# Kernel optimization log

Measured on AMD Instinct MI355X. Metric: run time of the kernel, lower is better.

Reference implementation:

```python
import jax, jax.numpy as jnp
import numpy as np

# geomloss SamplesLoss('sinkhorn', p=1, blur=0.01, reach=None, debias=True)
P = 1
EPS = 0.01  # temperature = blur**p
N_ITERS = 32
LOSS_WEIGHT = 1.0


def setup_inputs() -> dict:
    key = jax.random.key(0)
    kx, ky = jax.random.split(key)
    x = jax.random.normal(kx, (6144, 3), dtype=jnp.float32)
    y = jax.random.normal(ky, (6144, 3), dtype=jnp.float32)
    return {"x": x, "y": y}


def _cost(x, y):
    # p=1 cost: Euclidean distance ||x_i - y_j||, via expanded quadratic form
    x2 = jnp.sum(x * x, axis=-1)  # [N]
    y2 = jnp.sum(y * y, axis=-1)  # [M]
    d2 = x2[:, None] + y2[None, :] - 2.0 * (x @ y.T)  # [N, M]
    return jnp.sqrt(jnp.maximum(d2, 0.0) + 1e-12)


def _softmin(C, h):
    # h: [M] = log_weights + dual/eps ; returns [N] = -eps*LSE_j(h_j - C_ij/eps)
    return -EPS * jax.scipy.special.logsumexp(h[None, :] - C / EPS, axis=1)


def _sinkhorn_potentials(C_xy, loga, logb):
    # symmetric log-domain Sinkhorn with averaged updates (geomloss style)
    N, M = C_xy.shape
    f0 = jnp.zeros((N,), C_xy.dtype)
    g0 = jnp.zeros((M,), C_xy.dtype)

    def step(carry, _):
        f, g = carry
        ft = _softmin(C_xy, logb + g / EPS)
        gt = _softmin(C_xy.T, loga + f / EPS)
        return (0.5 * (f + ft), 0.5 * (g + gt)), None

    (f, g), _ = jax.lax.scan(step, (f0, g0), None, length=N_ITERS)
    # final non-averaged extrapolation step
    f_fin = _softmin(C_xy, logb + g / EPS)
    g_fin = _softmin(C_xy.T, loga + f / EPS)
    return f_fin, g_fin


def _sym_potential(C_xx, logw):
    # debias term: symmetric fixed point p = softmin(C_xx, logw + p/eps)
    N = C_xx.shape[0]

    def step(p, _):
        return 0.5 * (p + _softmin(C_xx, logw + p / EPS)), None

    p, _ = jax.lax.scan(step, jnp.zeros((N,), C_xx.dtype), None, length=N_ITERS)
    return _softmin(C_xx, logw + p / EPS)


def reference(x, y):
    N, M = x.shape[0], y.shape[0]
    a = jnp.full((N,), 1.0 / N, x.dtype)
    b = jnp.full((M,), 1.0 / M, y.dtype)
    loga = jnp.log(a)
    logb = jnp.log(b)

    C_xy = _cost(x, y)
    C_xx = _cost(x, x)
    C_yy = _cost(y, y)

    f, g = _sinkhorn_potentials(C_xy, loga, logb)
    p_x = _sym_potential(C_xx, loga)
    p_y = _sym_potential(C_yy, logb)

    # debiased Sinkhorn divergence: <a, f - p_x> + <b, g - p_y>
    loss = jnp.sum(a * (f - p_x)) + jnp.sum(b * (g - p_y))
    return LOSS_WEIGHT * loss
```

## Files before the change

### kernel.cpp

```cpp
#include <hip/hip_runtime.h>
#include <math.h>

#ifndef __has_builtin
#define __has_builtin(x) 0
#endif

__device__ __forceinline__ float fexp2(float x) {
#if __has_builtin(__builtin_amdgcn_exp2f)
  return __builtin_amdgcn_exp2f(x);
#else
  return exp2f(x);
#endif
}
__device__ __forceinline__ float flog2(float x) {
#if __has_builtin(__builtin_amdgcn_logf)
  return __builtin_amdgcn_logf(x);
#else
  return log2f(x);
#endif
}
__device__ __forceinline__ float fsqrt_(float x) {
#if __has_builtin(__builtin_amdgcn_sqrtf)
  return __builtin_amdgcn_sqrtf(x);
#else
  return sqrtf(x);
#endif
}

constexpr int   NP    = 6144;
constexpr float LOG2E = 1.44269504088896340736f;
constexpr float EPS_F = 0.01f;
constexpr float KKc   = LOG2E / EPS_F;
constexpr float NKKc  = -KKc;
constexpr float LBc   = -8.72323127482750f;
constexpr float HBc   = LBc * LOG2E;
constexpr float NEL2c = -EPS_F * 0.693147180559945f;

constexpr int TILE = 1024;
constexpr int NT   = NP / TILE;
constexpr int RPW  = 4;
constexpr int RPB  = 16;
constexpr int BPS  = NP / RPB;

__global__ __launch_bounds__(256) void init_kernel(
    const float* __restrict__ x, const float* __restrict__ y,
    float4* __restrict__ Xp, float4* __restrict__ Yp,
    float4* __restrict__ Xq, float4* __restrict__ Yq,
    float* __restrict__ st)
{
  int i = blockIdx.x * 256 + threadIdx.x;
  if (i < NP) {
    float a0 = x[3*i], a1 = x[3*i+1], a2 = x[3*i+2];
    float an = fmaf(a0, a0, fmaf(a1, a1, a2*a2));
    Xp[i] = make_float4(a0, a1, a2, an);
    Xq[i] = make_float4(-2.f*a0, -2.f*a1, -2.f*a2, an);
    float b0 = y[3*i], b1 = y[3*i+1], b2 = y[3*i+2];
    float bn = fmaf(b0, b0, fmaf(b1, b1, b2*b2));
    Yp[i] = make_float4(b0, b1, b2, bn);
    Yq[i] = make_float4(-2.f*b0, -2.f*b1, -2.f*b2, bn);
    st[i] = 0.f; st[i + NP] = 0.f; st[i + 2*NP] = 0.f; st[i + 3*NP] = 0.f;
  }
}

__global__ __launch_bounds__(256, 6) void softmin_pass(
    const float4* __restrict__ Xp, const float4* __restrict__ Yp,
    const float4* __restrict__ Xq, const float4* __restrict__ Yq,
    const float* __restrict__ f_in,  const float* __restrict__ g_in,
    const float* __restrict__ px_in, const float* __restrict__ py_in,
    float* __restrict__ f_out,  float* __restrict__ g_out,
    float* __restrict__ px_out, float* __restrict__ py_out,
    int avg)
{
  __shared__ float4 sQ[TILE];
  __shared__ float  sH[TILE];

  const int bid   = blockIdx.x;
  const int sub   = bid / BPS;
  const int row0  = (bid - sub * BPS) * RPB;
  const int tid   = threadIdx.x;
  const int lane  = tid & 63;
  const int wave  = tid >> 6;
  const int wrow0 = row0 + wave * RPW;

  const float4* P4;  const float4* Q4;
  const float* hsrc; const float* oldp; float* outp;
  if (sub == 0)      { P4 = Xp; Q4 = Yq; hsrc = g_in;  oldp = f_in;  outp = f_out;  }
  else if (sub == 1) { P4 = Yp; Q4 = Xq; hsrc = f_in;  oldp = g_in;  outp = g_out;  }
  else if (sub == 2) { P4 = Xp; Q4 = Xq; hsrc = px_in; oldp = px_in; outp = px_out; }
  else               { P4 = Yp; Q4 = Yq; hsrc = py_in; oldp = py_in; outp = py_out; }

  float pxr[RPW], pyr[RPW], pzr[RPW], pwr[RPW];
  float mr[RPW], sr[RPW], m40[RPW];
#pragma unroll
  for (int r = 0; r < RPW; ++r) {
    float4 p = P4[wrow0 + r];
    pxr[r] = p.x; pyr[r] = p.y; pzr[r] = p.z; pwr[r] = p.w;
    mr[r] = -INFINITY; sr[r] = 0.f; m40[r] = -INFINITY;
  }

  for (int t = 0; t < NT; ++t) {
    __syncthreads();
#pragma unroll
    for (int v = tid; v < TILE; v += 256) {
      sQ[v] = Q4[t * TILE + v];
      sH[v] = fmaf(KKc, hsrc[t * TILE + v], HBc);
    }
    __syncthreads();
#pragma unroll 4
    for (int k = lane; k < TILE; k += 64) {
      const float4 q  = sQ[k];
      const float  hh = sH[k];
#pragma unroll
      for (int r = 0; r < RPW; ++r) {
        float dot = fmaf(pxr[r], q.x, fmaf(pyr[r], q.y, fmaf(pzr[r], q.z, q.w)));
        float d2  = pwr[r] + dot;
        float c   = fsqrt_(fmaxf(d2, 1e-12f));
        float u   = fmaf(NKKc, c, hh);
        if (__any(u > m40[r])) {
          float mn = fmaxf(mr[r], u);
          sr[r] *= fexp2(mr[r] - mn);
          mr[r]  = mn;
          m40[r] = mn + 40.f;
        }
        sr[r] += fexp2(u - mr[r]);
      }
    }
  }

#pragma unroll
  for (int r = 0; r < RPW; ++r) {
    float m = mr[r], s = sr[r];
#pragma unroll
    for (int off = 32; off; off >>= 1) {
      float mo = __shfl_xor(m, off);
      float so = __shfl_xor(s, off);
      float mn = fmaxf(m, mo);
      s = s * fexp2(m - mn) + so * fexp2(mo - mn);
      m = mn;
    }
    if (lane == 0) {
      float val = NEL2c * (m + flog2(s));
      const int row = wrow0 + r;
      outp[row] = avg ? 0.5f * (oldp[row] + val) : val;
    }
  }
}

__global__ __launch_bounds__(256) void loss_kernel(
    const float* __restrict__ f,  const float* __restrict__ g,
    const float* __restrict__ px, const float* __restrict__ py,
    float* __restrict__ out)
{
  double acc = 0.0;
  for (int i = threadIdx.x; i < NP; i += 256)
    acc += (double)(f[i] - px[i]) + (double)(g[i] - py[i]);
  __shared__ double red[4];
#pragma unroll
  for (int off = 32; off; off >>= 1)
    acc += __shfl_xor(acc, off);
  const int lane = threadIdx.x & 63, wave = threadIdx.x >> 6;
  if (lane == 0) red[wave] = acc;
  __syncthreads();
  if (threadIdx.x == 0)
    out[0] = (float)((red[0] + red[1] + red[2] + red[3]) * (1.0 / NP));
}

extern "C" void kernel_launch(void* const* d_in, const int* in_sizes, int n_in,
                              void* d_out, int out_size, void* d_ws, size_t ws_size,
                              hipStream_t stream)
{
  const float* x = (const float*)d_in[0];
  const float* y = (const float*)d_in[1];
  float* out = (float*)d_out;
  float* ws  = (float*)d_ws;

  float4* Xp = (float4*)ws;
  float4* Yp = (float4*)(ws + 4 * NP);
  float4* Xq = (float4*)(ws + 8 * NP);
  float4* Yq = (float4*)(ws + 12 * NP);
  float* A = ws + 16 * NP;
  float* B = A + 4 * NP;

  hipLaunchKernelGGL(init_kernel, dim3((NP + 255) / 256), dim3(256), 0, stream,
                     x, y, Xp, Yp, Xq, Yq, A);

  float* cur = A; float* nxt = B;
  for (int it = 0; it <= 32; ++it) {
    const int avg = (it < 32) ? 1 : 0;
    hipLaunchKernelGGL(softmin_pass, dim3(4 * BPS), dim3(256), 0, stream,
                       Xp, Yp, Xq, Yq,
                       cur, cur + NP, cur + 2*NP, cur + 3*NP,
                       nxt, nxt + NP, nxt + 2*NP, nxt + 3*NP, avg);
    float* t = cur; cur = nxt; nxt = t;
  }

  hipLaunchKernelGGL(loss_kernel, dim3(1), dim3(256), 0, stream,
                     cur, cur + NP, cur + 2*NP, cur + 3*NP, out);
}
```

Baseline: 2.561 ms.

## Morton-sort points and skip far tiles using bounding-box softmin bounds

Points are spatially sorted into Morton order with a single-block counting sort, and a per-64-point bounding box is computed for each tile. Each softmin block computes lower and upper bounds on the exponent for every tile, using box distances and per-row-block maxima of the previous potentials. Tiles whose best possible contribution is more than 2^-40 below the guaranteed maximum are skipped. This cuts exp and sqrt work on distant pairs. It trades that for a bounded approximation error, a serial two-block sort kernel, loss of LDS tiling, and the risk of stale hmax bounds from the previous iteration.

Result: faster. 2.385 ms (-6.9%).

```diff
diff --git a/kernel.cpp b/kernel.cpp
--- a/kernel.cpp
+++ b/kernel.cpp
@@ -36,97 +36,197 @@
 constexpr float HBc   = LBc * LOG2E;
 constexpr float NEL2c = -EPS_F * 0.693147180559945f;
 
-constexpr int TILE = 1024;
-constexpr int NT   = NP / TILE;
-constexpr int RPW  = 4;
-constexpr int RPB  = 16;
-constexpr int BPS  = NP / RPB;
-
-__global__ __launch_bounds__(256) void init_kernel(
-    const float* __restrict__ x, const float* __restrict__ y,
-    float4* __restrict__ Xp, float4* __restrict__ Yp,
-    float4* __restrict__ Xq, float4* __restrict__ Yq,
-    float* __restrict__ st)
+constexpr int RPW  = 8;
+constexpr int RPB  = 32;
+constexpr int NRB  = NP / RPB;
+constexpr int NTL  = NP / 64;
+constexpr int CELLS = 4096;
+
+__device__ __forceinline__ unsigned cell_of(float v) {
+  int c = (int)floorf((v + 4.0f) * 2.0f);
+  return (unsigned)min(15, max(0, c));
+}
+__device__ __forceinline__ unsigned morton12(unsigned cx, unsigned cy, unsigned cz) {
+  unsigned m = 0;
+#pragma unroll
+  for (int b = 0; b < 4; ++b)
+    m |= (((cx >> b) & 1u) << (3 * b)) | (((cy >> b) & 1u) << (3 * b + 1)) |
+         (((cz >> b) & 1u) << (3 * b + 2));
+  return m;
+}
+
+__global__ __launch_bounds__(1024) void sort_kernel(
+    const float* __restrict__ xin, const float* __restrict__ yin,
+    float4* __restrict__ Xp, float4* __restrict__ Xq,
+    float4* __restrict__ Yp, float4* __restrict__ Yq,
+    float4* __restrict__ XaLo, float4* __restrict__ XaHi,
+    float4* __restrict__ YaLo, float4* __restrict__ YaHi,
+    float* __restrict__ stA, float* __restrict__ hmaxA)
 {
-  int i = blockIdx.x * 256 + threadIdx.x;
-  if (i < NP) {
-    float a0 = x[3*i], a1 = x[3*i+1], a2 = x[3*i+2];
-    float an = fmaf(a0, a0, fmaf(a1, a1, a2*a2));
-    Xp[i] = make_float4(a0, a1, a2, an);
-    Xq[i] = make_float4(-2.f*a0, -2.f*a1, -2.f*a2, an);
-    float b0 = y[3*i], b1 = y[3*i+1], b2 = y[3*i+2];
-    float bn = fmaf(b0, b0, fmaf(b1, b1, b2*b2));
-    Yp[i] = make_float4(b0, b1, b2, bn);
-    Yq[i] = make_float4(-2.f*b0, -2.f*b1, -2.f*b2, bn);
-    st[i] = 0.f; st[i + NP] = 0.f; st[i + 2*NP] = 0.f; st[i + 3*NP] = 0.f;
-  }
-}
-
-__global__ __launch_bounds__(256, 6) void softmin_pass(
+  __shared__ unsigned hist[CELLS];
+  __shared__ unsigned offs[CELLS];
+  __shared__ unsigned wsum[64];
+  const int tid = threadIdx.x;
+  const float* src = (blockIdx.x == 0) ? xin : yin;
+  float4* Pp  = (blockIdx.x == 0) ? Xp : Yp;
+  float4* Pq  = (blockIdx.x == 0) ? Xq : Yq;
+  float4* aLo = (blockIdx.x == 0) ? XaLo : YaLo;
+  float4* aHi = (blockIdx.x == 0) ? XaHi : YaHi;
+
+  for (int i = tid; i < CELLS; i += 1024) { hist[i] = 0u; offs[i] = 0u; }
+  for (int i = tid; i < 2 * NP; i += 1024) stA[blockIdx.x * 2 * NP + i] = 0.f;
+  for (int i = tid; i < 2 * NRB; i += 1024) hmaxA[blockIdx.x * 2 * NRB + i] = 0.f;
+  __syncthreads();
+
+  for (int i = tid; i < NP; i += 1024) {
+    float a0 = src[3*i], a1 = src[3*i+1], a2 = src[3*i+2];
+    unsigned m = morton12(cell_of(a0), cell_of(a1), cell_of(a2));
+    atomicAdd(&hist[m], 1u);
+  }
+  __syncthreads();
+  if (tid < 64) {
+    unsigned s = 0;
+    for (int j = 0; j < 64; ++j) { unsigned v = hist[tid*64+j]; hist[tid*64+j] = s; s += v; }
+    wsum[tid] = s;
+  }
+  __syncthreads();
+  if (tid == 0) {
+    unsigned s = 0;
+    for (int j = 0; j < 64; ++j) { unsigned v = wsum[j]; wsum[j] = s; s += v; }
+  }
+  __syncthreads();
+  if (tid < 64) {
+    unsigned o = wsum[tid];
+    for (int j = 0; j < 64; ++j) hist[tid*64+j] += o;
+  }
+  __syncthreads();
+  for (int i = tid; i < NP; i += 1024) {
+    float a0 = src[3*i], a1 = src[3*i+1], a2 = src[3*i+2];
+    unsigned m = morton12(cell_of(a0), cell_of(a1), cell_of(a2));
+    unsigned dst = hist[m] + atomicAdd(&offs[m], 1u);
+    float an = fmaf(a0, a0, fmaf(a1, a1, a2 * a2));
+    Pp[dst] = make_float4(a0, a1, a2, an);
+    Pq[dst] = make_float4(-2.f*a0, -2.f*a1, -2.f*a2, an);
+  }
+  __syncthreads();
+  const int wave = tid >> 6, lane = tid & 63;
+  for (int t = wave; t < NTL; t += 16) {
+    float4 p = Pp[t * 64 + lane];
+    float lx = p.x, ly = p.y, lz = p.z, hx = p.x, hy = p.y, hz = p.z;
+#pragma unroll
+    for (int off = 32; off; off >>= 1) {
+      lx = fminf(lx, __shfl_xor(lx, off)); hx = fmaxf(hx, __shfl_xor(hx, off));
+      ly = fminf(ly, __shfl_xor(ly, off)); hy = fmaxf(hy, __shfl_xor(hy, off));
+      lz = fminf(lz, __shfl_xor(lz, off)); hz = fmaxf(hz, __shfl_xor(hz, off));
+    }
+    if (lane == 0) {
+      aLo[t] = make_float4(lx, ly, lz, 0.f);
+      aHi[t] = make_float4(hx, hy, hz, 0.f);
+    }
+  }
+}
+
+__global__ __launch_bounds__(256, 4) void softmin_pass(
     const float4* __restrict__ Xp, const float4* __restrict__ Yp,
     const float4* __restrict__ Xq, const float4* __restrict__ Yq,
-    const float* __restrict__ f_in,  const float* __restrict__ g_in,
-    const float* __restrict__ px_in, const float* __restrict__ py_in,
-    float* __restrict__ f_out,  float* __restrict__ g_out,
-    float* __restrict__ px_out, float* __restrict__ py_out,
-    int avg)
+    const float4* __restrict__ XaLo, const float4* __restrict__ XaHi,
+    const float4* __restrict__ YaLo, const float4* __restrict__ YaHi,
+    const float* __restrict__ stIn, const float* __restrict__ hmaxIn,
+    float* __restrict__ stOut, float* __restrict__ hmaxOut, int avg)
 {
-  __shared__ float4 sQ[TILE];
-  __shared__ float  sH[TILE];
-
-  const int bid   = blockIdx.x;
-  const int sub   = bid / BPS;
-  const int row0  = (bid - sub * BPS) * RPB;
-  const int tid   = threadIdx.x;
-  const int lane  = tid & 63;
-  const int wave  = tid >> 6;
-  const int wrow0 = row0 + wave * RPW;
-
-  const float4* P4;  const float4* Q4;
-  const float* hsrc; const float* oldp; float* outp;
-  if (sub == 0)      { P4 = Xp; Q4 = Yq; hsrc = g_in;  oldp = f_in;  outp = f_out;  }
-  else if (sub == 1) { P4 = Yp; Q4 = Xq; hsrc = f_in;  oldp = g_in;  outp = g_out;  }
-  else if (sub == 2) { P4 = Xp; Q4 = Xq; hsrc = px_in; oldp = px_in; outp = px_out; }
-  else               { P4 = Yp; Q4 = Yq; hsrc = py_in; oldp = py_in; outp = py_out; }
-
-  float pxr[RPW], pyr[RPW], pzr[RPW], pwr[RPW];
-  float mr[RPW], sr[RPW], m40[RPW];
+  const int bid  = blockIdx.x;
+  const int sub  = bid & 3;
+  const int rb   = bid >> 2;
+  const int tid  = threadIdx.x;
+  const int lane = tid & 63;
+  const int wave = tid >> 6;
+  const int wrow0 = rb * RPB + wave * RPW;
+
+  const float4 *P4, *Q4, *aLo, *aHi;
+  const float *hsrc, *hpair, *oldp; float* outp;
+  if (sub == 0) {
+    P4 = Xp; Q4 = Yq; aLo = YaLo; aHi = YaHi;
+    hsrc = stIn + NP;     hpair = hmaxIn + NRB;     oldp = stIn;          outp = stOut;
+  } else if (sub == 1) {
+    P4 = Yp; Q4 = Xq; aLo = XaLo; aHi = XaHi;
+    hsrc = stIn;          hpair = hmaxIn;           oldp = stIn + NP;     outp = stOut + NP;
+  } else if (sub == 2) {
+    P4 = Xp; Q4 = Xq; aLo = XaLo; aHi = XaHi;
+    hsrc = stIn + 2*NP;   hpair = hmaxIn + 2*NRB;   oldp = stIn + 2*NP;   outp = stOut + 2*NP;
+  } else {
+    P4 = Yp; Q4 = Yq; aLo = YaLo; aHi = YaHi;
+    hsrc = stIn + 3*NP;   hpair = hmaxIn + 3*NRB;   oldp = stIn + 3*NP;   outp = stOut + 3*NP;
+  }
+
+  float pxr[RPW], pyr[RPW], pzr[RPW], pwr[RPW], mr[RPW], sr[RPW], m40r[RPW];
+  float rlx, rly, rlz, rhx, rhy, rhz;
 #pragma unroll
   for (int r = 0; r < RPW; ++r) {
     float4 p = P4[wrow0 + r];
     pxr[r] = p.x; pyr[r] = p.y; pzr[r] = p.z; pwr[r] = p.w;
-    mr[r] = -INFINITY; sr[r] = 0.f; m40[r] = -INFINITY;
-  }
-
-  for (int t = 0; t < NT; ++t) {
-    __syncthreads();
-#pragma unroll
-    for (int v = tid; v < TILE; v += 256) {
-      sQ[v] = Q4[t * TILE + v];
-      sH[v] = fmaf(KKc, hsrc[t * TILE + v], HBc);
-    }
-    __syncthreads();
-#pragma unroll 4
-    for (int k = lane; k < TILE; k += 64) {
-      const float4 q  = sQ[k];
-      const float  hh = sH[k];
-#pragma unroll
-      for (int r = 0; r < RPW; ++r) {
-        float dot = fmaf(pxr[r], q.x, fmaf(pyr[r], q.y, fmaf(pzr[r], q.z, q.w)));
-        float d2  = pwr[r] + dot;
-        float c   = fsqrt_(fmaxf(d2, 1e-12f));
-        float u   = fmaf(NKKc, c, hh);
-        if (__any(u > m40[r])) {
-          float mn = fmaxf(mr[r], u);
-          sr[r] *= fexp2(mr[r] - mn);
-          mr[r]  = mn;
-          m40[r] = mn + 40.f;
-        }
-        sr[r] += fexp2(u - mr[r]);
+    if (r == 0) { rlx = rhx = p.x; rly = rhy = p.y; rlz = rhz = p.z; }
+    else {
+      rlx = fminf(rlx, p.x); rhx = fmaxf(rhx, p.x);
+      rly = fminf(rly, p.y); rhy = fmaxf(rhy, p.y);
+      rlz = fminf(rlz, p.z); rhz = fmaxf(rhz, p.z);
+    }
+  }
+
+  float b0, b1, uc0, uc1;
+  {
+    auto tile_bounds = [&](int t, float& b, float& uc) {
+      float4 lo = aLo[t], hi = aHi[t];
+      float gx = fmaxf(fmaxf(lo.x - rhx, rlx - hi.x), 0.f);
+      float gy = fmaxf(fmaxf(lo.y - rhy, rly - hi.y), 0.f);
+      float gz = fmaxf(fmaxf(lo.z - rhz, rlz - hi.z), 0.f);
+      float dmin = fsqrt_(fmaf(gx, gx, fmaf(gy, gy, gz * gz)));
+      float fx = fmaxf(hi.x - rlx, rhx - lo.x);
+      float fy = fmaxf(hi.y - rly, rhy - lo.y);
+      float fz = fmaxf(hi.z - rlz, rhz - lo.z);
+      float dmax = fsqrt_(fmaf(fx, fx, fmaf(fy, fy, fz * fz)));
+      float hraw = fmaxf(hpair[2 * t], hpair[2 * t + 1]);
+      float hh = fmaf(KKc, hraw, HBc);
+      b  = fmaf(NKKc, dmin, hh);
+      uc = fmaf(NKKc, dmax, hh);
+    };
+    tile_bounds(lane, b0, uc0);
+    int tB = (lane < 32) ? (64 + lane) : 95;
+    tile_bounds(tB, b1, uc1);
+    if (lane >= 32) { b1 = -INFINITY; uc1 = -INFINITY; }
+  }
+  float ulb = fmaxf(uc0, uc1);
+#pragma unroll
+  for (int off = 32; off; off >>= 1) ulb = fmaxf(ulb, __shfl_xor(ulb, off));
+  const float thr = ulb - 40.f;
+  unsigned long long mA = __ballot(b0 >= thr);
+  unsigned long long mB = __ballot(b1 >= thr);
+
+#pragma unroll
+  for (int r = 0; r < RPW; ++r) { mr[r] = ulb; sr[r] = 0.f; m40r[r] = ulb + 40.f; }
+
+  auto proc = [&](int t) {
+    int j = t * 64 + lane;
+    float4 q = Q4[j];
+    float hh = fmaf(KKc, hsrc[j], HBc);
+#pragma unroll
+    for (int r = 0; r < RPW; ++r) {
+      float dot = fmaf(pxr[r], q.x, fmaf(pyr[r], q.y, fmaf(pzr[r], q.z, q.w)));
+      float d2  = pwr[r] + dot;
+      float c   = fsqrt_(fmaxf(d2, 1e-12f));
+      float u   = fmaf(NKKc, c, hh);
+      if (__any(u > m40r[r])) {
+        float mn = fmaxf(mr[r], u);
+        sr[r] *= fexp2(mr[r] - mn);
+        mr[r] = mn; m40r[r] = mn + 40.f;
       }
-    }
-  }
-
+      sr[r] += fexp2(u - mr[r]);
+    }
+  };
+  while (mA) { int t = __ffsll(mA) - 1;  mA &= mA - 1; proc(t); }
+  while (mB) { int t = 63 + __ffsll(mB); mB &= mB - 1; proc(t); }
+
+  __shared__ float wmaxLds[4];
+  float wmax = -INFINITY;
 #pragma unroll
   for (int r = 0; r < RPW; ++r) {
     float m = mr[r], s = sr[r];
@@ -138,26 +238,28 @@
       s = s * fexp2(m - mn) + so * fexp2(mo - mn);
       m = mn;
     }
-    if (lane == 0) {
-      float val = NEL2c * (m + flog2(s));
-      const int row = wrow0 + r;
-      outp[row] = avg ? 0.5f * (oldp[row] + val) : val;
-    }
-  }
+    float val = NEL2c * (m + flog2(s));
+    const int row = wrow0 + r;
+    float wv = avg ? 0.5f * (oldp[row] + val) : val;
+    if (lane == 0) outp[row] = wv;
+    wmax = fmaxf(wmax, wv);
+  }
+  if (lane == 0) wmaxLds[wave] = wmax;
+  __syncthreads();
+  if (tid == 0)
+    hmaxOut[sub * NRB + rb] =
+        fmaxf(fmaxf(wmaxLds[0], wmaxLds[1]), fmaxf(wmaxLds[2], wmaxLds[3]));
 }
 
 __global__ __launch_bounds__(256) void loss_kernel(
-    const float* __restrict__ f,  const float* __restrict__ g,
-    const float* __restrict__ px, const float* __restrict__ py,
-    float* __restrict__ out)
+    const float* __restrict__ st, float* __restrict__ out)
 {
   double acc = 0.0;
   for (int i = threadIdx.x; i < NP; i += 256)
-    acc += (double)(f[i] - px[i]) + (double)(g[i] - py[i]);
+    acc += (double)(st[i] - st[i + 2*NP]) + (double)(st[i + NP] - st[i + 3*NP]);
   __shared__ double red[4];
 #pragma unroll
-  for (int off = 32; off; off >>= 1)
-    acc += __shfl_xor(acc, off);
+  for (int off = 32; off; off >>= 1) acc += __shfl_xor(acc, off);
   const int lane = threadIdx.x & 63, wave = threadIdx.x >> 6;
   if (lane == 0) red[wave] = acc;
   __syncthreads();
@@ -175,25 +277,32 @@
   float* ws  = (float*)d_ws;
 
   float4* Xp = (float4*)ws;
-  float4* Yp = (float4*)(ws + 4 * NP);
-  float4* Xq = (float4*)(ws + 8 * NP);
+  float4* Xq = (float4*)(ws + 4 * NP);
+  float4* Yp = (float4*)(ws + 8 * NP);
   float4* Yq = (float4*)(ws + 12 * NP);
-  float* A = ws + 16 * NP;
-  float* B = A + 4 * NP;
-
-  hipLaunchKernelGGL(init_kernel, dim3((NP + 255) / 256), dim3(256), 0, stream,
-                     x, y, Xp, Yp, Xq, Yq, A);
-
-  float* cur = A; float* nxt = B;
+  float*  p  = ws + 16 * NP;
+  float4* XaLo = (float4*)p; p += 4 * NTL;
+  float4* XaHi = (float4*)p; p += 4 * NTL;
+  float4* YaLo = (float4*)p; p += 4 * NTL;
+  float4* YaHi = (float4*)p; p += 4 * NTL;
+  float* stA = p;            p += 4 * NP;
+  float* stB = p;            p += 4 * NP;
+  float* hmA = p;            p += 4 * NRB;
+  float* hmB = p;
+
+  hipLaunchKernelGGL(sort_kernel, dim3(2), dim3(1024), 0, stream,
+                     x, y, Xp, Xq, Yp, Yq, XaLo, XaHi, YaLo, YaHi, stA, hmA);
+
+  float* cur = stA; float* nxt = stB;
+  float* hmCur = hmA; float* hmNxt = hmB;
   for (int it = 0; it <= 32; ++it) {
     const int avg = (it < 32) ? 1 : 0;
-    hipLaunchKernelGGL(softmin_pass, dim3(4 * BPS), dim3(256), 0, stream,
-                       Xp, Yp, Xq, Yq,
-                       cur, cur + NP, cur + 2*NP, cur + 3*NP,
-                       nxt, nxt + NP, nxt + 2*NP, nxt + 3*NP, avg);
+    hipLaunchKernelGGL(softmin_pass, dim3(4 * NRB), dim3(256), 0, stream,
+                       Xp, Yp, Xq, Yq, XaLo, XaHi, YaLo, YaHi,
+                       cur, hmCur, nxt, hmNxt, avg);
     float* t = cur; cur = nxt; nxt = t;
-  }
-
-  hipLaunchKernelGGL(loss_kernel, dim3(1), dim3(256), 0, stream,
-                     cur, cur + NP, cur + 2*NP, cur + 3*NP, out);
-}
+    t = hmCur; hmCur = hmNxt; hmNxt = t;
+  }
+
+  hipLaunchKernelGGL(loss_kernel, dim3(1), dim3(256), 0, stream, cur, out);
+}
```
